# Optimization experiments

Measured on AMD Instinct MI355X. Metric: run time of the kernel, lower is better.

## Reference

```python
import jax, jax.numpy as jnp
import numpy as np

LN_EPS = 1e-5


def setup_inputs() -> dict:
    key = jax.random.key(0)
    ks = jax.random.split(key, 8)
    B, DIM = 65536, 768
    feat = jax.random.normal(ks[0], (B, 2, DIM), dtype=jnp.float32)
    s = 1.0 / np.sqrt(DIM)
    W_int = jax.random.uniform(ks[1], (9, DIM), minval=-s, maxval=s, dtype=jnp.float32)
    W_stim = jax.random.uniform(ks[2], (9, DIM), minval=-s, maxval=s, dtype=jnp.float32)
    trans = jax.random.uniform(ks[3], (9, 9, 9), dtype=jnp.float32)  # torch.rand init
    ln_w = jnp.ones((9,), dtype=jnp.float32)
    ln_b = jnp.zeros((9,), dtype=jnp.float32)
    so = 1.0 / np.sqrt(18)
    W_out = jax.random.uniform(ks[4], (9, 18), minval=-so, maxval=so, dtype=jnp.float32)
    b_out = jax.random.uniform(ks[5], (9,), minval=-so, maxval=so, dtype=jnp.float32)
    return {"feat": feat, "W_int": W_int, "W_stim": W_stim, "trans": trans,
            "ln_w": ln_w, "ln_b": ln_b, "W_out": W_out, "b_out": b_out}


def reference(feat, W_int, W_stim, trans, ln_w, ln_b, W_out, b_out):
    # last_feat = intensity(feat[:,0,:]); this_feat = stimulation(feat[:,1,:])
    last = feat[:, 0, :] @ W_int.T   # [B, 9]
    this = feat[:, 1, :] @ W_stim.T  # [B, 9]
    # per-sample: temp[a,k] = sum_j last[j]*trans[a,j,k]; out[k] = sum_a this[a]*temp[a,k]
    # batched trilinear contraction replaces the Python loop:
    bil = jnp.einsum('ba,bj,ajk->bk', this, last, trans)  # [B, 9]
    # LayerNorm(9)
    mu = jnp.mean(bil, axis=-1, keepdims=True)
    var = jnp.mean(jnp.square(bil - mu), axis=-1, keepdims=True)
    ln = (bil - mu) * jax.lax.rsqrt(var + LN_EPS) * ln_w + ln_b
    cat = jnp.concatenate([this, ln], axis=1)  # [B, 18]
    return cat @ W_out.T + b_out  # [B, 9]
```

## Files before the change

kernel.cpp:

```cpp
#include <hip/hip_runtime.h>

#define LN_EPS 1e-5f

constexpr int DIM    = 768;
constexpr int NSPLIT = 4;
constexpr int BLOCK  = NSPLIT * 64;
constexpr int SEG    = DIM / NSPLIT;
constexpr int C      = 32;
constexpr int NCHUNK = SEG / C;

__launch_bounds__(BLOCK, 4)
__global__ void fused_concat_linear(const float* __restrict__ feat,
                                    const float* __restrict__ W_int,
                                    const float* __restrict__ W_stim,
                                    const float* __restrict__ trans,
                                    const float* __restrict__ ln_w,
                                    const float* __restrict__ ln_b,
                                    const float* __restrict__ W_out,
                                    const float* __restrict__ b_out,
                                    float* __restrict__ out,
                                    int B)
{
    __shared__ float sP[NSPLIT][18][64];

    const int lane = threadIdx.x & 63;
    const int wave = __builtin_amdgcn_readfirstlane(threadIdx.x >> 6);

    const int row = blockIdx.x * 64 + lane;
    const int rr  = min(row, B - 1);
    const float* frow = feat + (size_t)rr * (2 * DIM);

    float accL[9], accT[9];
#pragma unroll
    for (int a = 0; a < 9; ++a) { accL[a] = 0.f; accT[a] = 0.f; }

#pragma unroll
    for (int ch = 0; ch < NCHUNK; ++ch) {
        const int c0 = wave * SEG + ch * C;

        float4 f0[8], f1[8];
#pragma unroll
        for (int m = 0; m < 8; ++m) f0[m] = *(const float4*)(frow + c0 + 4 * m);
#pragma unroll
        for (int m = 0; m < 8; ++m) f1[m] = *(const float4*)(frow + DIM + c0 + 4 * m);

#pragma unroll
        for (int a = 0; a < 9; ++a) {
            const float* wi = W_int  + a * DIM + c0;
            const float* ws = W_stim + a * DIM + c0;
            float sL = accL[a];
#pragma unroll
            for (int m = 0; m < 8; ++m) {
                const float4 w = *(const float4*)(wi + 4 * m);
                sL = fmaf(f0[m].x, w.x, sL);
                sL = fmaf(f0[m].y, w.y, sL);
                sL = fmaf(f0[m].z, w.z, sL);
                sL = fmaf(f0[m].w, w.w, sL);
            }
            accL[a] = sL;
            float sT = accT[a];
#pragma unroll
            for (int m = 0; m < 8; ++m) {
                const float4 w = *(const float4*)(ws + 4 * m);
                sT = fmaf(f1[m].x, w.x, sT);
                sT = fmaf(f1[m].y, w.y, sT);
                sT = fmaf(f1[m].z, w.z, sT);
                sT = fmaf(f1[m].w, w.w, sT);
            }
            accT[a] = sT;
        }
    }

#pragma unroll
    for (int a = 0; a < 9; ++a) {
        sP[wave][a][lane]     = accL[a];
        sP[wave][9 + a][lane] = accT[a];
    }
    __syncthreads();

    if (wave == 0) {
        float lastv[9], thisv[9];
#pragma unroll
        for (int a = 0; a < 9; ++a) {
            lastv[a] = ((sP[0][a][lane]     + sP[1][a][lane])
                      + (sP[2][a][lane]     + sP[3][a][lane]));
            thisv[a] = ((sP[0][9 + a][lane] + sP[1][9 + a][lane])
                      + (sP[2][9 + a][lane] + sP[3][9 + a][lane]));
        }

        float bil[9];
#pragma unroll
        for (int k = 0; k < 9; ++k) bil[k] = 0.f;
#pragma unroll
        for (int a = 0; a < 9; ++a) {
#pragma unroll
            for (int j = 0; j < 9; ++j) {
                const float p = thisv[a] * lastv[j];
                const float* tp = trans + (a * 81 + j * 9);
#pragma unroll
                for (int k = 0; k < 9; ++k) bil[k] = fmaf(p, tp[k], bil[k]);
            }
        }

        float mu = 0.f;
#pragma unroll
        for (int k = 0; k < 9; ++k) mu += bil[k];
        mu *= (1.f / 9.f);
        float var = 0.f;
#pragma unroll
        for (int k = 0; k < 9; ++k) { const float d = bil[k] - mu; var = fmaf(d, d, var); }
        var *= (1.f / 9.f);
        const float rs = rsqrtf(var + LN_EPS);

        float lnv[9];
#pragma unroll
        for (int j = 0; j < 9; ++j)
            lnv[j] = fmaf((bil[j] - mu) * rs, ln_w[j], ln_b[j]);

        if (row < B) {
#pragma unroll
            for (int i = 0; i < 9; ++i) {
                float o = b_out[i];
#pragma unroll
                for (int a = 0; a < 9; ++a) o = fmaf(thisv[a], W_out[i * 18 + a], o);
#pragma unroll
                for (int j = 0; j < 9; ++j) o = fmaf(lnv[j], W_out[i * 18 + 9 + j], o);
                out[(size_t)row * 9 + i] = o;
            }
        }
    }
}

extern "C" void kernel_launch(void* const* d_in, const int* in_sizes, int n_in,
                              void* d_out, int out_size, void* d_ws, size_t ws_size,
                              hipStream_t stream) {
    const float* feat   = (const float*)d_in[0];
    const float* W_int  = (const float*)d_in[1];
    const float* W_stim = (const float*)d_in[2];
    const float* trans  = (const float*)d_in[3];
    const float* ln_w   = (const float*)d_in[4];
    const float* ln_b   = (const float*)d_in[5];
    const float* W_out  = (const float*)d_in[6];
    const float* b_out  = (const float*)d_in[7];
    float* out = (float*)d_out;

    const int B = in_sizes[0] / (2 * DIM);
    const int grid = (B + 63) / 64;

    fused_concat_linear<<<grid, BLOCK, 0, stream>>>(
        feat, W_int, W_stim, trans, ln_w, ln_b, W_out, b_out, out, B);
}
```

Baseline: 561.0 us.

## Stage feature loads through LDS with direct global-to-LDS async loads

Replaces the register-staged float4 loads of feature rows with `__builtin_amdgcn_global_load_lds`, which writes each lane's 16 bytes straight into a per-wave LDS buffer. Each lane then reads its own data back with ds_reads. The chunk width drops from 32 to 16 and the chunk loop is no longer unrolled. The aim is to cut VGPR pressure and let the hardware move data asynchronously into LDS. In exchange, every chunk waits for all outstanding loads with no double buffering, so fewer memory requests are in flight. It also adds 32KB of LDS per block and an extra LDS round trip per element.

```diff
diff --git a/kernel.cpp b/kernel.cpp
--- a/kernel.cpp
+++ b/kernel.cpp
@@ -6,8 +6,15 @@
 constexpr int NSPLIT = 4;
 constexpr int BLOCK  = NSPLIT * 64;
 constexpr int SEG    = DIM / NSPLIT;
-constexpr int C      = 32;
-constexpr int NCHUNK = SEG / C;
+constexpr int C      = 16;
+constexpr int NCH    = SEG / C;
+constexpr int WBUF   = 2 * C * 64;
+
+#define WAIT_VM0   0x0F70
+#define WAIT_LGKM0 0xC07F
+
+typedef const __attribute__((address_space(1))) void* gas_ptr;
+typedef __attribute__((address_space(3))) void*       las_ptr;
 
 __launch_bounds__(BLOCK, 4)
 __global__ void fused_concat_linear(const float* __restrict__ feat,
@@ -21,7 +28,7 @@
                                     float* __restrict__ out,
                                     int B)
 {
-    __shared__ float sP[NSPLIT][18][64];
+    __shared__ float lds[NSPLIT * WBUF];
 
     const int lane = threadIdx.x & 63;
     const int wave = __builtin_amdgcn_readfirstlane(threadIdx.x >> 6);
@@ -30,51 +37,55 @@
     const int rr  = min(row, B - 1);
     const float* frow = feat + (size_t)rr * (2 * DIM);
 
+    float* wbuf = lds + wave * WBUF;
+
     float accL[9], accT[9];
 #pragma unroll
     for (int a = 0; a < 9; ++a) { accL[a] = 0.f; accT[a] = 0.f; }
 
-#pragma unroll
-    for (int ch = 0; ch < NCHUNK; ++ch) {
+    for (int ch = 0; ch < NCH; ++ch) {
         const int c0 = wave * SEG + ch * C;
 
-        float4 f0[8], f1[8];
 #pragma unroll
-        for (int m = 0; m < 8; ++m) f0[m] = *(const float4*)(frow + c0 + 4 * m);
-#pragma unroll
-        for (int m = 0; m < 8; ++m) f1[m] = *(const float4*)(frow + DIM + c0 + 4 * m);
+        for (int m = 0; m < 4; ++m) {
+            __builtin_amdgcn_global_load_lds((gas_ptr)(frow + c0 + 4 * m),
+                                             (las_ptr)(wbuf + m * 256), 16, 0, 0);
+            __builtin_amdgcn_global_load_lds((gas_ptr)(frow + DIM + c0 + 4 * m),
+                                             (las_ptr)(wbuf + 1024 + m * 256), 16, 0, 0);
+        }
+        __builtin_amdgcn_s_waitcnt(WAIT_VM0);
 
 #pragma unroll
-        for (int a = 0; a < 9; ++a) {
-            const float* wi = W_int  + a * DIM + c0;
-            const float* ws = W_stim + a * DIM + c0;
-            float sL = accL[a];
+        for (int m = 0; m < 4; ++m) {
+            const float4 x0 = *(const float4*)(wbuf + m * 256 + 4 * lane);
+            const float4 x1 = *(const float4*)(wbuf + 1024 + m * 256 + 4 * lane);
 #pragma unroll
-            for (int m = 0; m < 8; ++m) {
-                const float4 w = *(const float4*)(wi + 4 * m);
-                sL = fmaf(f0[m].x, w.x, sL);
-                sL = fmaf(f0[m].y, w.y, sL);
-                sL = fmaf(f0[m].z, w.z, sL);
-                sL = fmaf(f0[m].w, w.w, sL);
+            for (int a = 0; a < 9; ++a) {
+                const float4 w0 = *(const float4*)(W_int + a * DIM + c0 + 4 * m);
+                float sL = accL[a];
+                sL = fmaf(x0.x, w0.x, sL);
+                sL = fmaf(x0.y, w0.y, sL);
+                sL = fmaf(x0.z, w0.z, sL);
+                sL = fmaf(x0.w, w0.w, sL);
+                accL[a] = sL;
+                const float4 w1 = *(const float4*)(W_stim + a * DIM + c0 + 4 * m);
+                float sT = accT[a];
+                sT = fmaf(x1.x, w1.x, sT);
+                sT = fmaf(x1.y, w1.y, sT);
+                sT = fmaf(x1.z, w1.z, sT);
+                sT = fmaf(x1.w, w1.w, sT);
+                accT[a] = sT;
             }
-            accL[a] = sL;
-            float sT = accT[a];
-#pragma unroll
-            for (int m = 0; m < 8; ++m) {
-                const float4 w = *(const float4*)(ws + 4 * m);
-                sT = fmaf(f1[m].x, w.x, sT);
-                sT = fmaf(f1[m].y, w.y, sT);
-                sT = fmaf(f1[m].z, w.z, sT);
-                sT = fmaf(f1[m].w, w.w, sT);
-            }
-            accT[a] = sT;
         }
+        __builtin_amdgcn_s_waitcnt(WAIT_LGKM0);
     }
 
+    __syncthreads();
+    float* sP = lds;
 #pragma unroll
     for (int a = 0; a < 9; ++a) {
-        sP[wave][a][lane]     = accL[a];
-        sP[wave][9 + a][lane] = accT[a];
+        sP[(wave * 18 + a) * 64 + lane]     = accL[a];
+        sP[(wave * 18 + 9 + a) * 64 + lane] = accT[a];
     }
     __syncthreads();
 
@@ -82,10 +93,10 @@
         float lastv[9], thisv[9];
 #pragma unroll
         for (int a = 0; a < 9; ++a) {
-            lastv[a] = ((sP[0][a][lane]     + sP[1][a][lane])
-                      + (sP[2][a][lane]     + sP[3][a][lane]));
-            thisv[a] = ((sP[0][9 + a][lane] + sP[1][9 + a][lane])
-                      + (sP[2][9 + a][lane] + sP[3][9 + a][lane]));
+            lastv[a] = (sP[(0 * 18 + a) * 64 + lane] + sP[(1 * 18 + a) * 64 + lane])
+                     + (sP[(2 * 18 + a) * 64 + lane] + sP[(3 * 18 + a) * 64 + lane]);
+            thisv[a] = (sP[(0 * 18 + 9 + a) * 64 + lane] + sP[(1 * 18 + 9 + a) * 64 + lane])
+                     + (sP[(2 * 18 + 9 + a) * 64 + lane] + sP[(3 * 18 + 9 + a) * 64 + lane]);
         }
 
         float bil[9];
```

Measured after the change: 607.8 us. 8.3% more time.
